# Kernel tuning notes

Hardware: AMD Instinct MI355X
Metric: run time of the kernel (lower is better)

The kernel has to match this reference:

```python
import jax, jax.numpy as jnp
import numpy as np

D_IN = 1024
D_OUT = 1024
NUM_HEADS = 16
HEAD_DIM = D_OUT // NUM_HEADS


def setup_inputs() -> dict:
    key = jax.random.key(0)
    k1, k2, k3, k4 = jax.random.split(key, 4)
    x = jax.random.normal(k1, (2, 2048, D_IN), dtype=jnp.float32)
    # qkv Linear (bias=False): weight [3*d_out, d_in]
    w_qkv = jax.random.normal(k2, (3 * D_OUT, D_IN), dtype=jnp.float32) * (1.0 / np.sqrt(D_IN))
    # proj Linear (default bias=True): weight [d_out, d_out], bias [d_out]
    w_proj = jax.random.normal(k3, (D_OUT, D_OUT), dtype=jnp.float32) * (1.0 / np.sqrt(D_OUT))
    b_proj = jax.random.normal(k4, (D_OUT,), dtype=jnp.float32) * 0.01
    return {"x": x, "w_qkv": w_qkv, "w_proj": w_proj, "b_proj": b_proj}


def reference(x, w_qkv, w_proj, b_proj):
    B, S, E = x.shape
    qkv = jnp.einsum("bse,fe->bsf", x, w_qkv)                 # [B,S,3*d_out]
    qkv = qkv.reshape(B, S, 3, NUM_HEADS, HEAD_DIM)
    qkv = jnp.transpose(qkv, (2, 0, 3, 1, 4))                  # [3,B,H,S,D]
    q, k, v = qkv[0], qkv[1], qkv[2]
    scores = jnp.einsum("bhqd,bhkd->bhqk", q, k)               # [B,H,S,S]
    causal = jnp.triu(jnp.ones((S, S), dtype=bool), k=1)
    scores = jnp.where(causal, -jnp.inf, scores)
    # NOTE: source divides by head_dim**(-0.5), i.e. multiplies by sqrt(head_dim)
    scores = scores / (HEAD_DIM ** -0.5)
    attn = jax.nn.softmax(scores, axis=-1)
    ctx = jnp.einsum("bhqk,bhkd->bhqd", attn, v)               # [B,H,S,D]
    ctx = jnp.transpose(ctx, (0, 2, 1, 3)).reshape(B, S, E)
    return jnp.einsum("bse,fe->bsf", ctx, w_proj) + b_proj
```

## Files before the change

### kernel.cpp

```cpp
#include <hip/hip_runtime.h>

typedef _Float16 f16;
typedef _Float16 f16x4 __attribute__((ext_vector_type(4)));
typedef _Float16 f16x8 __attribute__((ext_vector_type(8)));
typedef float f32x4 __attribute__((ext_vector_type(4)));

#define MFMA16(a, b, c) __builtin_amdgcn_mfma_f32_16x16x32_f16(a, b, c, 0, 0, 0)
#define QSCALE 11.5415603f

typedef const __attribute__((address_space(1))) void* gp1_t;
typedef __attribute__((address_space(3))) void* lp3_t;
__device__ __forceinline__ void gld16(const void* g, void* l) {
    __builtin_amdgcn_global_load_lds((gp1_t)g, (lp3_t)l, 16, 0, 0);
}

__global__ __launch_bounds__(256) void cvt_all(
    const float* __restrict__ x, const float* __restrict__ wq, const float* __restrict__ wp,
    f16* __restrict__ xh, f16* __restrict__ wqh, f16* __restrict__ wph)
{
    int i = blockIdx.x * 256 + threadIdx.x;
    const float4* src; f16x4* dst; int off;
    if (i < 1048576)      { src = (const float4*)x;  dst = (f16x4*)xh;  off = i; }
    else if (i < 1835008) { src = (const float4*)wq; dst = (f16x4*)wqh; off = i - 1048576; }
    else                  { src = (const float4*)wp; dst = (f16x4*)wph; off = i - 1835008; }
    float4 v = src[off];
    f16x4 o = { (f16)v.x, (f16)v.y, (f16)v.z, (f16)v.w };
    dst[off] = o;
}

template<int EPI, int BN>
__global__ __launch_bounds__(256) void gemm_k(
    const f16* __restrict__ A, const f16* __restrict__ B, int K,
    f16* __restrict__ qb, f16* __restrict__ kb, f16* __restrict__ vt,
    float* __restrict__ outF, const float* __restrict__ bias)
{
    __shared__ f16 as[128 * 32];
    __shared__ f16 bs[BN * 32];
    constexpr int WN = BN / 2;
    constexpr int NT = BN / 32;
    const int t = threadIdx.x;
    const int bidf = blockIdx.y * gridDim.x + blockIdx.x;
    const int cpx  = (gridDim.x * gridDim.y) >> 3;
    const int swz  = (bidf & 7) * cpx + (bidf >> 3);
    const int m0 = (swz / gridDim.x) * 128, n0 = (swz % gridDim.x) * BN;
    const int lane = t & 63, wv = t >> 6;
    const int wm = wv >> 1, wn = wv & 1;
    const int lr = lane & 15, g = lane >> 4;
    const int srow = lane >> 2, schk = (lane & 3) * 8;
    const f16* Ab = A + (size_t)m0 * K;
    const f16* Bb = B + (size_t)n0 * K;
    f32x4 acc[4][NT] = {};

    for (int k0 = 0; k0 < K; k0 += 32) {
        __syncthreads();
        #pragma unroll
        for (int i2 = 0; i2 < 2; ++i2) {
            const int r0 = wv * 32 + i2 * 16;
            gld16(&Ab[(size_t)(r0 + srow) * K + k0 + schk], &as[r0 * 32]);
        }
        if constexpr (BN == 128) {
            #pragma unroll
            for (int i2 = 0; i2 < 2; ++i2) {
                const int r0 = wv * 32 + i2 * 16;
                gld16(&Bb[(size_t)(r0 + srow) * K + k0 + schk], &bs[r0 * 32]);
            }
        } else {
            const int r0 = wv * 16;
            gld16(&Bb[(size_t)(r0 + srow) * K + k0 + schk], &bs[r0 * 32]);
        }
        __syncthreads();
        f16x8 af[4], bf[NT];
        #pragma unroll
        for (int mt = 0; mt < 4; ++mt)
            af[mt] = *reinterpret_cast<const f16x8*>(&as[(wm * 64 + mt * 16 + lr) * 32 + g * 8]);
        #pragma unroll
        for (int nt = 0; nt < NT; ++nt)
            bf[nt] = *reinterpret_cast<const f16x8*>(&bs[(wn * WN + nt * 16 + lr) * 32 + g * 8]);
        #pragma unroll
        for (int mt = 0; mt < 4; ++mt)
            #pragma unroll
            for (int nt = 0; nt < NT; ++nt)
                acc[mt][nt] = MFMA16(af[mt], bf[nt], acc[mt][nt]);
    }

    #pragma unroll
    for (int mt = 0; mt < 4; ++mt) {
        #pragma unroll
        for (int nt = 0; nt < NT; ++nt) {
            const int n = n0 + wn * WN + nt * 16 + lr;
            const int s0 = m0 + wm * 64 + mt * 16 + 4 * g;
            if (EPI == 0) {
                const int which = n >> 10, h = (n >> 6) & 15, d = n & 63;
                const int b = s0 >> 11, s = s0 & 2047;
                if (which == 2) {
                    f16x4 vv;
                    #pragma unroll
                    for (int i = 0; i < 4; ++i) vv[i] = (f16)acc[mt][nt][i];
                    *reinterpret_cast<f16x4*>(&vt[((size_t)((b << 4) + h) * 64 + d) * 2048 + s]) = vv;
                } else {
                    f16* dst = which ? kb : qb;
                    const float sc = which ? 1.0f : QSCALE;
                    #pragma unroll
                    for (int i = 0; i < 4; ++i)
                        dst[((size_t)((b << 4) + h) * 2048 + (s + i)) * 64 + d] = (f16)(acc[mt][nt][i] * sc);
                }
            } else {
                #pragma unroll
                for (int i = 0; i < 4; ++i)
                    outF[(size_t)(s0 + i) * 1024 + n] = acc[mt][nt][i] + bias[n];
            }
        }
    }
}

__global__ __launch_bounds__(64, 2) void attn_k(
    const f16* __restrict__ Q, const f16* __restrict__ K, const f16* __restrict__ VT,
    f16* __restrict__ ctx, f16* __restrict__ opart,
    float* __restrict__ mpart, float* __restrict__ lpart)
{
    __shared__ f16 lp[64][72];
    const int lane = threadIdx.x;
    const int lr = lane & 15, g = lane >> 4;
    const int bid = blockIdx.x;
    const int bh = bid & 31;
    const int rr = 67 - (bid >> 5);
    int u, c;
    if (rr < 10)      { u = rr;                 c = 0; }
    else if (rr < 30) { u = 10 + (rr - 10) / 2; c = (rr - 10) % 2; }
    else if (rr < 60) { u = 20 + (rr - 30) / 3; c = (rr - 30) % 3; }
    else              { u = 30 + (rr - 60) / 4; c = (rr - 60) % 4; }
    const int ntt = u + 1;
    const int nc  = 1 + u / 10;
    const int cbase = ntt / nc, crem = ntt % nc;
    const int start = c * cbase + (c < crem ? c : crem);
    const int len   = cbase + (c < crem ? 1 : 0);
    const bool diag = (start + len == ntt);

    const int b = bh >> 4, h = bh & 15;
    const size_t base = (size_t)bh * (2048 * 64);
    const f16* Qb = Q + base;
    const f16* Kb = K + base;
    const f16* Vb = VT + base;
    const int q0 = u << 6;

    f16x8 qf[4][2];
    #pragma unroll
    for (int nt = 0; nt < 4; ++nt)
        #pragma unroll
        for (int ks = 0; ks < 2; ++ks)
            qf[nt][ks] = *reinterpret_cast<const f16x8*>(&Qb[(size_t)(q0 + nt * 16 + lr) * 64 + ks * 32 + g * 8]);

    f32x4 o[4][4] = {};
    float mrun[4] = { -1e30f, -1e30f, -1e30f, -1e30f };
    float lsum[4] = { 0.f, 0.f, 0.f, 0.f };
    f16x8 akA[4][2], akB[4][2];

#define LOADK(BUF, I) do {                                                              \
    const int kvL_ = (start + (I)) << 6;                                                \
    _Pragma("unroll")                                                                   \
    for (int mt = 0; mt < 4; ++mt)                                                      \
        _Pragma("unroll")                                                               \
        for (int ks = 0; ks < 2; ++ks)                                                  \
            BUF[mt][ks] = *reinterpret_cast<const f16x8*>(                              \
                &Kb[(size_t)(kvL_ + mt * 16 + lr) * 64 + ks * 32 + g * 8]);             \
} while (0)

#define TILE_BODY(BUF, I, DIAGM) do {                                                   \
    const int kv0_ = (start + (I)) << 6;                                                \
    f32x4 st[4][4] = {};                                                                \
    _Pragma("unroll")                                                                   \
    for (int mt = 0; mt < 4; ++mt)                                                      \
        _Pragma("unroll")                                                               \
        for (int nt = 0; nt < 4; ++nt)                                                  \
            if (!(DIAGM) || mt <= nt) {                                                 \
                _Pragma("unroll")                                                       \
                for (int ks = 0; ks < 2; ++ks)                                          \
                    st[mt][nt] = MFMA16(BUF[mt][ks], qf[nt][ks], st[mt][nt]);           \
            }                                                                           \
    _Pragma("unroll")                                                                   \
    for (int nt = 0; nt < 4; ++nt) {                                                    \
        float mloc = -1e30f;                                                            \
        _Pragma("unroll")                                                               \
        for (int mt = 0; mt < 4; ++mt) {                                                \
            if ((DIAGM) && mt > nt) continue;                                           \
            _Pragma("unroll")                                                           \
            for (int i = 0; i < 4; ++i) {                                               \
                float sv = st[mt][nt][i];                                               \
                if ((DIAGM) && mt == nt) {         \
                    sv = (4 * g + i <= lr) ? sv : -1e30f;                               \
                    st[mt][nt][i] = sv;                                                 \
                }                                                                       \
                mloc = fmaxf(mloc, sv);                                                 \
            }                                                                           \
        }                                                                               \
        mloc = fmaxf(mloc, __shfl_xor(mloc, 16));                                       \
        mloc = fmaxf(mloc, __shfl_xor(mloc, 32));                                       \
        if (__any(mloc > mrun[nt] + 8.0f)) {                             \
            float mnew = fmaxf(mrun[nt], mloc);                                         \
            float sc = exp2f(mrun[nt] - mnew);                                          \
            lsum[nt] *= sc;                                                             \
            _Pragma("unroll")                                                           \
            for (int mo = 0; mo < 4; ++mo)                                              \
                _Pragma("unroll")                                                       \
                for (int i = 0; i < 4; ++i) o[mo][nt][i] *= sc;                         \
            mrun[nt] = mnew;                                                            \
        }                                                                               \
        float ls = 0.f;                                                                 \
        _Pragma("unroll")                                                               \
        for (int mt = 0; mt < 4; ++mt) {                                                \
            f16x4 pk;                                                                   \
            if ((DIAGM) && mt > nt) {                                                   \
                pk[0] = pk[1] = pk[2] = pk[3] = (f16)0.f;                               \
            } else {                                                                    \
                _Pragma("unroll")                                                       \
                for (int i = 0; i < 4; ++i) {                                           \
                    float p = exp2f(st[mt][nt][i] - mrun[nt]);                          \
                    ls += p; pk[i] = (f16)p;                                            \
                }                                                                       \
            }                                                                           \
            *reinterpret_cast<f16x4*>(&lp[nt * 16 + lr][mt * 16 + 4 * g]) = pk;         \
        }                                                                               \
        lsum[nt] += ls;                                                                 \
    }                                                                                   \
    {                                                                                   \
        f16x8 pf[4][2];                                                                 \
        _Pragma("unroll")                                                               \
        for (int nt = 0; nt < 4; ++nt)                                                  \
            _Pragma("unroll")                                                           \
            for (int ks = 0; ks < 2; ++ks)                                              \
                pf[nt][ks] = *reinterpret_cast<const f16x8*>(                           \
                    &lp[nt * 16 + lr][ks * 32 + g * 8]);                                \
        _Pragma("unroll")                                                               \
        for (int mo = 0; mo < 4; ++mo) {                                                \
            f16x8 av[2];                                                                \
            _Pragma("unroll")                                                           \
            for (int ks = 0; ks < 2; ++ks)                                              \
                av[ks] = *reinterpret_cast<const f16x8*>(                               \
                    &Vb[(size_t)(mo * 16 + lr) * 2048 + kv0_ + ks * 32 + g * 8]);       \
            _Pragma("unroll")                                                           \
            for (int nt = 0; nt < 4; ++nt)                                              \
                _Pragma("unroll")                                                       \
                for (int ks = 0; ks < 2; ++ks)                                          \
                    o[mo][nt] = MFMA16(av[ks], pf[nt][ks], o[mo][nt]);                  \
        }                                                                               \
    }                                                                                   \
} while (0)

    const int nfull = len - (diag ? 1 : 0);
    LOADK(akA, 0);
    int i = 0;
    for (; i + 2 <= nfull; i += 2) {
        LOADK(akB, i + 1);
        TILE_BODY(akA, i, 0);
        if (i + 2 < len) LOADK(akA, i + 2);
        TILE_BODY(akB, i + 1, 0);
    }
    if (i < nfull) {
        if (diag) {
            LOADK(akB, i + 1);
            TILE_BODY(akA, i, 0);
            TILE_BODY(akB, i + 1, 1);
        } else {
            TILE_BODY(akA, i, 0);
        }
    } else if (diag) {
        TILE_BODY(akA, nfull, 1);
    }
#undef LOADK
#undef TILE_BODY

    const bool split = (nc > 1);
    int slot = 0;
    if (split) {
        const int psl = (u < 20) ? 2 * (u - 10) : (u < 30 ? 20 + 3 * (u - 20) : 50 + 4 * (u - 30));
        slot = bh * 58 + psl + c;
    }
    #pragma unroll
    for (int nt = 0; nt < 4; ++nt) {
        float l = lsum[nt];
        l += __shfl_xor(l, 16);
        l += __shfl_xor(l, 32);
        const float inv = 1.0f / l;
        const int lrow = nt * 16 + lr;
        if (!split) {
            const size_t rowoff = ((size_t)(b * 2048 + q0 + lrow)) * 1024 + h * 64;
            #pragma unroll
            for (int mo = 0; mo < 4; ++mo) {
                f16x4 ov;
                #pragma unroll
                for (int i2 = 0; i2 < 4; ++i2) ov[i2] = (f16)(o[mo][nt][i2] * inv);
                *reinterpret_cast<f16x4*>(&ctx[rowoff + mo * 16 + 4 * g]) = ov;
            }
        } else {
            const int mi = slot * 64 + lrow;
            #pragma unroll
            for (int mo = 0; mo < 4; ++mo) {
                f16x4 ov;
                #pragma unroll
                for (int i2 = 0; i2 < 4; ++i2) ov[i2] = (f16)(o[mo][nt][i2] * inv);
                *reinterpret_cast<f16x4*>(&opart[(size_t)mi * 64 + mo * 16 + 4 * g]) = ov;
            }
            if (g == 0) { mpart[mi] = mrun[nt]; lpart[mi] = l; }
        }
    }
}

__global__ __launch_bounds__(256) void combine_k(
    const f16* __restrict__ opart, const float* __restrict__ mpart,
    const float* __restrict__ lpart, f16* __restrict__ ctx)
{
    const int blk = blockIdx.x;
    const int bh = blk & 31, u = 10 + (blk >> 5);
    const int b = bh >> 4, h = bh & 15;
    const int nc = 1 + u / 10;
    const int psl = (u < 20) ? 2 * (u - 10) : (u < 30 ? 20 + 3 * (u - 20) : 50 + 4 * (u - 30));
    const int slot0 = bh * 58 + psl;
    const int t = threadIdx.x;
    const int lrow = t >> 2, seg = t & 3;

    float m[4], l[4], w[4];
    float M = -1e30f;
    #pragma unroll 4
    for (int cc = 0; cc < 4; ++cc) if (cc < nc) {
        m[cc] = mpart[(slot0 + cc) * 64 + lrow];
        l[cc] = lpart[(slot0 + cc) * 64 + lrow];
        M = fmaxf(M, m[cc]);
    }
    float wsum = 0.f;
    #pragma unroll 4
    for (int cc = 0; cc < 4; ++cc) if (cc < nc) { w[cc] = l[cc] * exp2f(m[cc] - M); wsum += w[cc]; }
    const float r = 1.0f / wsum;

    float acc[16] = {};
    #pragma unroll 4
    for (int cc = 0; cc < 4; ++cc) if (cc < nc) {
        const float coef = w[cc] * r;
        const size_t rb = (size_t)((slot0 + cc) * 64 + lrow) * 64 + seg * 16;
        f16x8 v0 = *reinterpret_cast<const f16x8*>(&opart[rb]);
        f16x8 v1 = *reinterpret_cast<const f16x8*>(&opart[rb + 8]);
        #pragma unroll
        for (int i = 0; i < 8; ++i) { acc[i] += coef * (float)v0[i]; acc[i + 8] += coef * (float)v1[i]; }
    }
    f16x8 o0, o1;
    #pragma unroll
    for (int i = 0; i < 8; ++i) { o0[i] = (f16)acc[i]; o1[i] = (f16)acc[i + 8]; }
    const size_t wb = ((size_t)(b * 2048 + u * 64 + lrow)) * 1024 + h * 64 + seg * 16;
    *reinterpret_cast<f16x8*>(&ctx[wb]) = o0;
    *reinterpret_cast<f16x8*>(&ctx[wb + 8]) = o1;
}

extern "C" void kernel_launch(void* const* d_in, const int* in_sizes, int n_in,
                              void* d_out, int out_size, void* d_ws, size_t ws_size,
                              hipStream_t stream) {
    const float* x      = (const float*)d_in[0];
    const float* w_qkv  = (const float*)d_in[1];
    const float* w_proj = (const float*)d_in[2];
    const float* b_proj = (const float*)d_in[3];
    float* out = (float*)d_out;

    char* p = (char*)d_ws;
    f16* xh     = (f16*)p; p += (size_t)4096 * 1024 * 2;
    f16* wqkvh  = (f16*)p; p += (size_t)3072 * 1024 * 2;
    f16* wprojh = (f16*)p; p += (size_t)1024 * 1024 * 2;
    f16* qbuf   = (f16*)p; p += (size_t)2 * 16 * 2048 * 64 * 2;
    f16* kbuf   = (f16*)p; p += (size_t)2 * 16 * 2048 * 64 * 2;
    f16* vtbuf  = (f16*)p; p += (size_t)2 * 16 * 64 * 2048 * 2;
    f16* ctx    = (f16*)p; p += (size_t)4096 * 1024 * 2;

    f16*   opart = (f16*)d_out;
    float* mpart = (float*)xh;
    float* lpart = mpart + 118784;

    cvt_all<<<8192, 256, 0, stream>>>(x, w_qkv, w_proj, xh, wqkvh, wprojh);

    gemm_k<0, 128><<<dim3(24, 32), 256, 0, stream>>>(xh, wqkvh, 1024, qbuf, kbuf, vtbuf, nullptr, nullptr);

    attn_k<<<2176, 64, 0, stream>>>(qbuf, kbuf, vtbuf, ctx, opart, mpart, lpart);

    combine_k<<<704, 256, 0, stream>>>(opart, mpart, lpart, ctx);

    gemm_k<1, 64><<<dim3(16, 32), 256, 0, stream>>>(ctx, wprojh, 1024, nullptr, nullptr, nullptr, out, b_proj);
}
```

Before: 196.4 us.

## Share K/V tiles across four query-tile waves via LDS double buffering

Attention blocks now hold four waves, each owning one 64-row query tile of a four-tile group. K and V tiles are staged once per block into double-buffered, XOR-swizzled LDS through global_load_lds and shared by all four waves, where before each single-wave block loaded K and V directly from global memory. The KV split scheme and the combine kernel are reworked around the new grouping, with splits of 3 only for the later groups. Waves whose causal range ends earlier sit idle at the barriers, and the larger blocks cut the number of blocks launched.

```diff
diff --git a/kernel.cpp b/kernel.cpp
--- a/kernel.cpp
+++ b/kernel.cpp
@@ -113,35 +113,41 @@
     }
 }
 
-__global__ __launch_bounds__(64, 2) void attn_k(
+__global__ __launch_bounds__(256) void attn_k(
     const f16* __restrict__ Q, const f16* __restrict__ K, const f16* __restrict__ VT,
     f16* __restrict__ ctx, f16* __restrict__ opart,
     float* __restrict__ mpart, float* __restrict__ lpart)
 {
-    __shared__ f16 lp[64][72];
-    const int lane = threadIdx.x;
+    __shared__ f16 kbuf[2][64 * 64];
+    __shared__ f16 vbuf[2][64 * 64];
+    __shared__ f16 lp[4][64][72];
+    const int t = threadIdx.x, wv = t >> 6, lane = t & 63;
     const int lr = lane & 15, g = lane >> 4;
     const int bid = blockIdx.x;
     const int bh = bid & 31;
-    const int rr = 67 - (bid >> 5);
-    int u, c;
-    if (rr < 10)      { u = rr;                 c = 0; }
-    else if (rr < 30) { u = 10 + (rr - 10) / 2; c = (rr - 10) % 2; }
-    else if (rr < 60) { u = 20 + (rr - 30) / 3; c = (rr - 30) % 3; }
-    else              { u = 30 + (rr - 60) / 4; c = (rr - 60) % 4; }
-    const int ntt = u + 1;
-    const int nc  = 1 + u / 10;
-    const int cbase = ntt / nc, crem = ntt % nc;
+    const int rest = bid >> 5;
+    int grp, c;
+    if (rest == 0)      { grp = 3; c = 0; }
+    else if (rest == 1) { grp = 2; c = 0; }
+    else if (rest < 8)  { grp = 7 - (rest - 2) / 3; c = (rest - 2) % 3; }
+    else if (rest == 8) { grp = 1; c = 0; }
+    else if (rest < 15) { grp = 5 - (rest - 9) / 3; c = (rest - 9) % 3; }
+    else                { grp = 0; c = 0; }
+    const int E  = 4 * grp + 4;
+    const int nc = (grp < 4) ? 1 : 3;
+    const int cbase = E / nc, crem = E % nc;
     const int start = c * cbase + (c < crem ? c : crem);
     const int len   = cbase + (c < crem ? 1 : 0);
-    const bool diag = (start + len == ntt);
+    const int end   = start + len;
+    const int uw = 4 * grp + wv;
+    const int q0 = uw << 6;
+    const int myEnd = (uw + 1 < end) ? (uw + 1) : end;
 
     const int b = bh >> 4, h = bh & 15;
     const size_t base = (size_t)bh * (2048 * 64);
     const f16* Qb = Q + base;
     const f16* Kb = K + base;
     const f16* Vb = VT + base;
-    const int q0 = u << 6;
 
     f16x8 qf[4][2];
     #pragma unroll
@@ -153,30 +159,45 @@
     f32x4 o[4][4] = {};
     float mrun[4] = { -1e30f, -1e30f, -1e30f, -1e30f };
     float lsum[4] = { 0.f, 0.f, 0.f, 0.f };
-    f16x8 akA[4][2], akB[4][2];
-
-#define LOADK(BUF, I) do {                                                              \
-    const int kvL_ = (start + (I)) << 6;                                                \
+
+    const int lrow8 = lane >> 3, lchk = lane & 7;
+
+#define STAGE(TT, BSEL) do {                                                            \
+    const int kv0s_ = (TT) << 6;                                                        \
+    f16* kd_ = &kbuf[BSEL][0];                                                          \
+    f16* vd_ = &vbuf[BSEL][0];                                                          \
     _Pragma("unroll")                                                                   \
-    for (int mt = 0; mt < 4; ++mt)                                                      \
-        _Pragma("unroll")                                                               \
-        for (int ks = 0; ks < 2; ++ks)                                                  \
-            BUF[mt][ks] = *reinterpret_cast<const f16x8*>(                              \
-                &Kb[(size_t)(kvL_ + mt * 16 + lr) * 64 + ks * 32 + g * 8]);             \
+    for (int i2 = 0; i2 < 2; ++i2) {                                                    \
+        const int rr = wv * 16 + i2 * 8;                     \
+        const int krow = rr + lrow8;                                                    \
+        gld16(&Kb[(size_t)(kv0s_ + krow) * 64 + ((lchk ^ (krow & 7)) * 8)],             \
+              kd_ + rr * 64);                                                           \
+        gld16(&Vb[(size_t)krow * 2048 + kv0s_ + ((lchk ^ (krow & 7)) * 8)],             \
+              vd_ + rr * 64);                                                           \
+    }                                                                                   \
 } while (0)
 
-#define TILE_BODY(BUF, I, DIAGM) do {                                                   \
-    const int kv0_ = (start + (I)) << 6;                                                \
+#define TILE_BODY(BSEL, KV0, DIAGM) do {                                                \
+    const int kv0_ = (KV0);                                                             \
+    const f16* kc_ = &kbuf[BSEL][0];                                                    \
+    const f16* vc_ = &vbuf[BSEL][0];                                                    \
     f32x4 st[4][4] = {};                                                                \
     _Pragma("unroll")                                                                   \
-    for (int mt = 0; mt < 4; ++mt)                                                      \
+    for (int mt = 0; mt < 4; ++mt) {                                                    \
+        const int r_ = mt * 16 + lr;                                                    \
+        f16x8 ak[2];                                                                    \
+        _Pragma("unroll")                                                               \
+        for (int ks = 0; ks < 2; ++ks)                                                  \
+            ak[ks] = *reinterpret_cast<const f16x8*>(                                   \
+                &kc_[r_ * 64 + ((4 * ks + g) ^ (lr & 7)) * 8]);                         \
         _Pragma("unroll")                                                               \
         for (int nt = 0; nt < 4; ++nt)                                                  \
             if (!(DIAGM) || mt <= nt) {                                                 \
                 _Pragma("unroll")                                                       \
                 for (int ks = 0; ks < 2; ++ks)                                          \
-                    st[mt][nt] = MFMA16(BUF[mt][ks], qf[nt][ks], st[mt][nt]);           \
+                    st[mt][nt] = MFMA16(ak[ks], qf[nt][ks], st[mt][nt]);                \
             }                                                                           \
+    }                                                                                   \
     _Pragma("unroll")                                                                   \
     for (int nt = 0; nt < 4; ++nt) {                                                    \
         float mloc = -1e30f;                                                            \
@@ -186,7 +207,7 @@
             _Pragma("unroll")                                                           \
             for (int i = 0; i < 4; ++i) {                                               \
                 float sv = st[mt][nt][i];                                               \
-                if ((DIAGM) && mt == nt) {         \
+                if ((DIAGM) && mt == nt) {                                              \
                     sv = (4 * g + i <= lr) ? sv : -1e30f;                               \
                     st[mt][nt][i] = sv;                                                 \
                 }                                                                       \
@@ -195,7 +216,7 @@
         }                                                                               \
         mloc = fmaxf(mloc, __shfl_xor(mloc, 16));                                       \
         mloc = fmaxf(mloc, __shfl_xor(mloc, 32));                                       \
-        if (__any(mloc > mrun[nt] + 8.0f)) {                             \
+        if (__any(mloc > mrun[nt] + 8.0f)) {                                            \
             float mnew = fmaxf(mrun[nt], mloc);                                         \
             float sc = exp2f(mrun[nt] - mnew);                                          \
             lsum[nt] *= sc;                                                             \
@@ -212,13 +233,14 @@
             if ((DIAGM) && mt > nt) {                                                   \
                 pk[0] = pk[1] = pk[2] = pk[3] = (f16)0.f;                               \
             } else {                                                                    \
-                _Pragma("unroll")                                                       \
-                for (int i = 0; i < 4; ++i) {                                           \
-                    float p = exp2f(st[mt][nt][i] - mrun[nt]);                          \
-                    ls += p; pk[i] = (f16)p;                                            \
-                }                                                                       \
+                float p0 = exp2f(st[mt][nt][0] - mrun[nt]);                             \
+                float p1 = exp2f(st[mt][nt][1] - mrun[nt]);                             \
+                float p2 = exp2f(st[mt][nt][2] - mrun[nt]);                             \
+                float p3 = exp2f(st[mt][nt][3] - mrun[nt]);                             \
+                ls += (p0 + p1) + (p2 + p3);                                            \
+                pk[0] = (f16)p0; pk[1] = (f16)p1; pk[2] = (f16)p2; pk[3] = (f16)p3;     \
             }                                                                           \
-            *reinterpret_cast<f16x4*>(&lp[nt * 16 + lr][mt * 16 + 4 * g]) = pk;         \
+            *reinterpret_cast<f16x4*>(&lp[wv][nt * 16 + lr][mt * 16 + 4 * g]) = pk;     \
         }                                                                               \
         lsum[nt] += ls;                                                                 \
     }                                                                                   \
@@ -229,14 +251,15 @@
             _Pragma("unroll")                                                           \
             for (int ks = 0; ks < 2; ++ks)                                              \
                 pf[nt][ks] = *reinterpret_cast<const f16x8*>(                           \
-                    &lp[nt * 16 + lr][ks * 32 + g * 8]);                                \
+                    &lp[wv][nt * 16 + lr][ks * 32 + g * 8]);                            \
         _Pragma("unroll")                                                               \
         for (int mo = 0; mo < 4; ++mo) {                                                \
+            const int d_ = mo * 16 + lr;                                                \
             f16x8 av[2];                                                                \
             _Pragma("unroll")                                                           \
             for (int ks = 0; ks < 2; ++ks)                                              \
                 av[ks] = *reinterpret_cast<const f16x8*>(                               \
-                    &Vb[(size_t)(mo * 16 + lr) * 2048 + kv0_ + ks * 32 + g * 8]);       \
+                    &vc_[d_ * 64 + ((4 * ks + g) ^ (lr & 7)) * 8]);                     \
             _Pragma("unroll")                                                           \
             for (int nt = 0; nt < 4; ++nt)                                              \
                 _Pragma("unroll")                                                       \
@@ -246,35 +269,27 @@
     }                                                                                   \
 } while (0)
 
-    const int nfull = len - (diag ? 1 : 0);
-    LOADK(akA, 0);
-    int i = 0;
-    for (; i + 2 <= nfull; i += 2) {
-        LOADK(akB, i + 1);
-        TILE_BODY(akA, i, 0);
-        if (i + 2 < len) LOADK(akA, i + 2);
-        TILE_BODY(akB, i + 1, 0);
-    }
-    if (i < nfull) {
-        if (diag) {
-            LOADK(akB, i + 1);
-            TILE_BODY(akA, i, 0);
-            TILE_BODY(akB, i + 1, 1);
-        } else {
-            TILE_BODY(akA, i, 0);
-        }
-    } else if (diag) {
-        TILE_BODY(akA, nfull, 1);
-    }
-#undef LOADK
+    if ((start & 1) == 0) STAGE(start, 0); else STAGE(start, 1);
+    __syncthreads();
+
+    for (int tt = start; tt < end; ++tt) {
+        const int cur = tt & 1;
+        if (tt + 1 < end) {
+            if (cur) STAGE(tt + 1, 0); else STAGE(tt + 1, 1);
+        }
+        if (tt < myEnd) {
+            if (tt == uw) {
+                if (cur) TILE_BODY(1, tt << 6, 1); else TILE_BODY(0, tt << 6, 1);
+            } else {
+                if (cur) TILE_BODY(1, tt << 6, 0); else TILE_BODY(0, tt << 6, 0);
+            }
+        }
+        __syncthreads();
+    }
+#undef STAGE
 #undef TILE_BODY
 
     const bool split = (nc > 1);
-    int slot = 0;
-    if (split) {
-        const int psl = (u < 20) ? 2 * (u - 10) : (u < 30 ? 20 + 3 * (u - 20) : 50 + 4 * (u - 30));
-        slot = bh * 58 + psl + c;
-    }
     #pragma unroll
     for (int nt = 0; nt < 4; ++nt) {
         float l = lsum[nt];
@@ -292,7 +307,8 @@
                 *reinterpret_cast<f16x4*>(&ctx[rowoff + mo * 16 + 4 * g]) = ov;
             }
         } else {
-            const int mi = slot * 64 + lrow;
+            const int slot = bh * 12 + (grp - 4) * 3 + c;
+            const int mi = slot * 256 + wv * 64 + lrow;
             #pragma unroll
             for (int mo = 0; mo < 4; ++mo) {
                 f16x4 ov;
@@ -310,32 +326,32 @@
     const float* __restrict__ lpart, f16* __restrict__ ctx)
 {
     const int blk = blockIdx.x;
-    const int bh = blk & 31, u = 10 + (blk >> 5);
+    const int bh = blk & 31, u = 16 + (blk >> 5);
     const int b = bh >> 4, h = bh & 15;
-    const int nc = 1 + u / 10;
-    const int psl = (u < 20) ? 2 * (u - 10) : (u < 30 ? 20 + 3 * (u - 20) : 50 + 4 * (u - 30));
-    const int slot0 = bh * 58 + psl;
+    const int grp = u >> 2;
+    const int slot0 = bh * 12 + (grp - 4) * 3;
+    const int rowbase = (u & 3) * 64;
     const int t = threadIdx.x;
     const int lrow = t >> 2, seg = t & 3;
 
-    float m[4], l[4], w[4];
+    float m[3], l[3], w[3];
     float M = -1e30f;
-    #pragma unroll 4
-    for (int cc = 0; cc < 4; ++cc) if (cc < nc) {
-        m[cc] = mpart[(slot0 + cc) * 64 + lrow];
-        l[cc] = lpart[(slot0 + cc) * 64 + lrow];
+    #pragma unroll
+    for (int cc = 0; cc < 3; ++cc) {
+        m[cc] = mpart[(slot0 + cc) * 256 + rowbase + lrow];
+        l[cc] = lpart[(slot0 + cc) * 256 + rowbase + lrow];
         M = fmaxf(M, m[cc]);
     }
     float wsum = 0.f;
-    #pragma unroll 4
-    for (int cc = 0; cc < 4; ++cc) if (cc < nc) { w[cc] = l[cc] * exp2f(m[cc] - M); wsum += w[cc]; }
+    #pragma unroll
+    for (int cc = 0; cc < 3; ++cc) { w[cc] = l[cc] * exp2f(m[cc] - M); wsum += w[cc]; }
     const float r = 1.0f / wsum;
 
     float acc[16] = {};
-    #pragma unroll 4
-    for (int cc = 0; cc < 4; ++cc) if (cc < nc) {
+    #pragma unroll
+    for (int cc = 0; cc < 3; ++cc) {
         const float coef = w[cc] * r;
-        const size_t rb = (size_t)((slot0 + cc) * 64 + lrow) * 64 + seg * 16;
+        const size_t rb = (size_t)((slot0 + cc) * 256 + rowbase + lrow) * 64 + seg * 16;
         f16x8 v0 = *reinterpret_cast<const f16x8*>(&opart[rb]);
         f16x8 v1 = *reinterpret_cast<const f16x8*>(&opart[rb + 8]);
         #pragma unroll
@@ -369,15 +385,15 @@
 
     f16*   opart = (f16*)d_out;
     float* mpart = (float*)xh;
-    float* lpart = mpart + 118784;
+    float* lpart = mpart + 98304;
 
     cvt_all<<<8192, 256, 0, stream>>>(x, w_qkv, w_proj, xh, wqkvh, wprojh);
 
     gemm_k<0, 128><<<dim3(24, 32), 256, 0, stream>>>(xh, wqkvh, 1024, qbuf, kbuf, vtbuf, nullptr, nullptr);
 
-    attn_k<<<2176, 64, 0, stream>>>(qbuf, kbuf, vtbuf, ctx, opart, mpart, lpart);
-
-    combine_k<<<704, 256, 0, stream>>>(opart, mpart, lpart, ctx);
+    attn_k<<<512, 256, 0, stream>>>(qbuf, kbuf, vtbuf, ctx, opart, mpart, lpart);
+
+    combine_k<<<512, 256, 0, stream>>>(opart, mpart, lpart, ctx);
 
     gemm_k<1, 64><<<dim3(16, 32), 256, 0, stream>>>(ctx, wprojh, 1024, nullptr, nullptr, nullptr, out, b_proj);
 }
```

Measured after the change: 216.5 us. 1.1x slower.
